# Kernel tuning notes

Hardware: AMD Instinct MI355X
Metric: run time of the kernel (lower is better)

The kernel has to match this reference:

```python
import jax, jax.numpy as jnp
import numpy as np
import math

B, T, O, D, H, L, FF = 2, 1024, 512, 1024, 16, 4, 4096
MAX_SEQ = 1024


def _ln(x, g, b, eps=1e-5):
    m = jnp.mean(x, -1, keepdims=True)
    v = jnp.mean((x - m) ** 2, -1, keepdims=True)
    return (x - m) * jax.lax.rsqrt(v + eps) * g + b


def _gelu(x):
    return jax.nn.gelu(x, approximate=False)  # torch nn.GELU default = exact erf


def setup_inputs() -> dict:
    key = jax.random.key(0)
    ks = iter(jax.random.split(key, 64))
    std = 0.02
    def w(shape):
        return (jax.random.normal(next(ks), shape, jnp.float32) * std)
    d = {
        'obs': jax.random.normal(next(ks), (B, T, O), jnp.float32),
        # encoder MLP: Linear(O,D), LN, GELU, Linear(D,D), GELU, Linear(D,D), LN
        'enc_w1': w((O, D)), 'enc_b1': jnp.zeros((D,)),
        'enc_g1': jnp.ones((D,)), 'enc_be1': jnp.zeros((D,)),
        'enc_w2': w((D, D)), 'enc_b2': jnp.zeros((D,)),
        'enc_w3': w((D, D)), 'enc_b3': jnp.zeros((D,)),
        'enc_g2': jnp.ones((D,)), 'enc_be2': jnp.zeros((D,)),
        'pos_emb': w((MAX_SEQ, D)),
        # stacked per-layer transformer params [L, ...]
        'ln1_g': jnp.ones((L, D)), 'ln1_b': jnp.zeros((L, D)),
        'wq': w((L, D, D)), 'bq': jnp.zeros((L, D)),
        'wk': w((L, D, D)), 'bk': jnp.zeros((L, D)),
        'wv': w((L, D, D)), 'bv': jnp.zeros((L, D)),
        'wo': w((L, D, D)), 'bo': jnp.zeros((L, D)),
        'ln2_g': jnp.ones((L, D)), 'ln2_b': jnp.zeros((L, D)),
        'mlp_w1': w((L, D, FF)), 'mlp_b1': jnp.zeros((L, FF)),
        'mlp_w2': w((L, FF, D)), 'mlp_b2': jnp.zeros((L, D)),
        'lnf_g': jnp.ones((D,)), 'lnf_b': jnp.zeros((D,)),
        'dec_w': w((D, O)), 'dec_b': jnp.zeros((O,)),
    }
    return d


def reference(obs, enc_w1, enc_b1, enc_g1, enc_be1, enc_w2, enc_b2, enc_w3, enc_b3,
              enc_g2, enc_be2, pos_emb, ln1_g, ln1_b, wq, bq, wk, bk, wv, bv, wo, bo,
              ln2_g, ln2_b, mlp_w1, mlp_b1, mlp_w2, mlp_b2, lnf_g, lnf_b, dec_w, dec_b):
    b, t, _ = obs.shape
    dh = D // H
    scale = 1.0 / math.sqrt(dh)
    # embedder MLP
    h = _gelu(_ln(obs @ enc_w1 + enc_b1, enc_g1, enc_be1))
    h = _gelu(h @ enc_w2 + enc_b2)
    h = _ln(h @ enc_w3 + enc_b3, enc_g2, enc_be2)
    x = h + pos_emb[:t]
    # causal mask [t, t]
    mask = jnp.tril(jnp.ones((t, t), bool))

    def block(x, p):
        g1, b1, Wq, Bq, Wk, Bk, Wv, Bv, Wo, Bo, g2, b2, W1, B1, W2, B2 = p
        hn = _ln(x, g1, b1)
        q = (hn @ Wq + Bq).reshape(b, t, H, dh).transpose(0, 2, 1, 3)
        k = (hn @ Wk + Bk).reshape(b, t, H, dh).transpose(0, 2, 1, 3)
        v = (hn @ Wv + Bv).reshape(b, t, H, dh).transpose(0, 2, 1, 3)
        att = jnp.einsum('bhtd,bhsd->bhts', q, k) * scale
        att = jnp.where(mask, att, -jnp.inf)
        att = jax.nn.softmax(att, axis=-1)
        y = jnp.einsum('bhts,bhsd->bhtd', att, v)
        y = y.transpose(0, 2, 1, 3).reshape(b, t, D)
        x = x + y @ Wo + Bo
        hm = _ln(x, g2, b2)
        x = x + _gelu(hm @ W1 + B1) @ W2 + B2
        return x, None

    stacked = (ln1_g, ln1_b, wq, bq, wk, bk, wv, bv, wo, bo,
               ln2_g, ln2_b, mlp_w1, mlp_b1, mlp_w2, mlp_b2)
    x, _ = jax.lax.scan(block, x, stacked)
    x = _ln(x, lnf_g, lnf_b)
    out_obs = x @ dec_w + dec_b
    return x, out_obs
```

## Files before the change

### kernel.cpp

```cpp
#include <hip/hip_runtime.h>

typedef unsigned short u16;
typedef __bf16  bf16x8 __attribute__((ext_vector_type(8)));
typedef float   f32x4  __attribute__((ext_vector_type(4)));
typedef unsigned short u16x4 __attribute__((ext_vector_type(4)));

constexpr int Bc = 2, Tc = 1024, Oc = 512, Dc = 1024, Hc = 16, Lc = 4, FFc = 4096;
constexpr int Mc = Bc * Tc;
constexpr int Sq = 3 * Dc;

__device__ __forceinline__ u16 f2b(float f) {
    unsigned u = __float_as_uint(f);
    u = (u + 0x7fffu + ((u >> 16) & 1u)) >> 16;
    return (u16)u;
}
__device__ __forceinline__ float gelu_f(float x) {
    return 0.5f * x * (1.0f + erff(x * 0.7071067811865476f));
}

__global__ __launch_bounds__(256) void wtrans(const float* __restrict__ in,
                                              u16* __restrict__ out, int R, int C,
                                              long inBatch, long outBatch) {
    __shared__ float t[32][33];
    const float* inp = in + (size_t)blockIdx.z * inBatch;
    u16* outp = out + (size_t)blockIdx.z * outBatch;
    const int tx = threadIdx.x & 31, ty = threadIdx.x >> 5;
    const int br = blockIdx.y * 32, bc = blockIdx.x * 32;
#pragma unroll
    for (int i = 0; i < 32; i += 8)
        t[ty + i][tx] = inp[(size_t)(br + ty + i) * C + bc + tx];
    __syncthreads();
#pragma unroll
    for (int i = 0; i < 32; i += 8)
        outp[(size_t)(bc + ty + i) * R + br + tx] = f2b(t[tx][ty + i]);
}

__global__ __launch_bounds__(256) void btrans(const u16* __restrict__ in,
                                              u16* __restrict__ out, int inStride) {
    __shared__ u16 t[32][33];
    const u16* inp = in + (size_t)blockIdx.z * Tc * inStride;
    u16* outp = out + (size_t)blockIdx.z * Dc * Tc;
    const int tx = threadIdx.x & 31, ty = threadIdx.x >> 5;
    const int br = blockIdx.y * 32, bc = blockIdx.x * 32;
#pragma unroll
    for (int i = 0; i < 32; i += 8)
        t[ty + i][tx] = inp[(size_t)(br + ty + i) * inStride + bc + tx];
    __syncthreads();
#pragma unroll
    for (int i = 0; i < 32; i += 8)
        outp[(size_t)(bc + ty + i) * Tc + br + tx] = t[tx][ty + i];
}

__global__ __launch_bounds__(256) void cvt_bf(const float* __restrict__ in,
                                              u16* __restrict__ out, int n) {
    int i = blockIdx.x * 256 + threadIdx.x;
    if (i * 4 >= n) return;
    float4 v = ((const float4*)in)[i];
    u16x4 r;
    r[0] = f2b(v.x); r[1] = f2b(v.y); r[2] = f2b(v.z); r[3] = f2b(v.w);
    ((u16x4*)out)[i] = r;
}

__global__ __launch_bounds__(256) void pack_qkv_bias(const float* __restrict__ bq,
    const float* __restrict__ bk, const float* __restrict__ bv, float* __restrict__ out) {
    int i = blockIdx.x * 256 + threadIdx.x;
    int l = i / Sq, j = i % Sq;
    float v = (j < Dc) ? bq[l * Dc + j] : (j < 2 * Dc ? bk[l * Dc + j - Dc] : bv[l * Dc + j - 2 * Dc]);
    out[i] = v;
}

__global__ __launch_bounds__(256) void ln_kernel(
    const float* __restrict__ in, const float* __restrict__ gam,
    const float* __restrict__ bet, const float* __restrict__ pos,
    float* __restrict__ outf, u16* __restrict__ outb, int do_gelu) {
    const int row = blockIdx.x, tid = threadIdx.x;
    const float4 v = ((const float4*)(in + (size_t)row * Dc))[tid];
    float s  = v.x + v.y + v.z + v.w;
    float ss = v.x * v.x + v.y * v.y + v.z * v.z + v.w * v.w;
#pragma unroll
    for (int m = 1; m < 64; m <<= 1) {
        s  += __shfl_xor(s,  m, 64);
        ss += __shfl_xor(ss, m, 64);
    }
    __shared__ float red[8];
    const int w = tid >> 6;
    if ((tid & 63) == 0) { red[w] = s; red[4 + w] = ss; }
    __syncthreads();
    s  = red[0] + red[1] + red[2] + red[3];
    ss = red[4] + red[5] + red[6] + red[7];
    const float mean = s * (1.0f / Dc);
    const float rstd = rsqrtf(ss * (1.0f / Dc) - mean * mean + 1e-5f);
    const float4 gv = ((const float4*)gam)[tid];
    const float4 bv = ((const float4*)bet)[tid];
    float y0 = (v.x - mean) * rstd * gv.x + bv.x;
    float y1 = (v.y - mean) * rstd * gv.y + bv.y;
    float y2 = (v.z - mean) * rstd * gv.z + bv.z;
    float y3 = (v.w - mean) * rstd * gv.w + bv.w;
    if (do_gelu) { y0 = gelu_f(y0); y1 = gelu_f(y1); y2 = gelu_f(y2); y3 = gelu_f(y3); }
    if (pos) {
        const float4 pv = ((const float4*)(pos + (size_t)(row & (Tc - 1)) * Dc))[tid];
        y0 += pv.x; y1 += pv.y; y2 += pv.z; y3 += pv.w;
    }
    if (outf) {
        float4 o; o.x = y0; o.y = y1; o.z = y2; o.w = y3;
        ((float4*)(outf + (size_t)row * Dc))[tid] = o;
    }
    if (outb) {
        u16x4 r; r[0] = f2b(y0); r[1] = f2b(y1); r[2] = f2b(y2); r[3] = f2b(y3);
        ((u16x4*)(outb + (size_t)row * Dc))[tid] = r;
    }
}

template<int BM, int BN, int FM, int FN, int WM, int WN, int OCC>
__global__ __launch_bounds__(256, OCC) void gemm_k(
    const u16* __restrict__ A, const u16* __restrict__ Bt,
    const float* __restrict__ bias, const float* resid,
    float* Cf, u16* Cb, int M, int N, int K, int do_gelu) {
    __shared__ u16 sA[2][BM][64];
    __shared__ u16 sB[2][BN][64];
    constexpr int NA = BM * 8 / 256;
    constexpr int NB = BN * 8 / 256;
    const int tid = threadIdx.x;
    const int lane = tid & 63, w = tid >> 6;
    const int lr = lane & 15, g = lane >> 4;
    const int wm = w / WN, wn = w % WN;

    const int gx = gridDim.x;
    const int nwg = gx * gridDim.y;
    const int orig = blockIdx.y * gx + blockIdx.x;
    const int wgid = (orig & 7) * (nwg >> 3) + (orig >> 3);
    const int bx = wgid % gx, by = wgid / gx;
    const long m0 = (long)by * BM, n0 = (long)bx * BN;

    const f32x4 fzero = {0.f, 0.f, 0.f, 0.f};
    f32x4 acc[FM][FN];
#pragma unroll
    for (int i = 0; i < FM; ++i)
#pragma unroll
        for (int j = 0; j < FN; ++j) acc[i][j] = fzero;

    bf16x8 ra[NA], rb[NB];
#pragma unroll
    for (int i = 0; i < NA; ++i) {
        int c = tid + 256 * i, row = c >> 3, cc = c & 7;
        ra[i] = *(const bf16x8*)(A + (size_t)(m0 + row) * K + cc * 8);
    }
#pragma unroll
    for (int i = 0; i < NB; ++i) {
        int c = tid + 256 * i, row = c >> 3, cc = c & 7;
        rb[i] = *(const bf16x8*)(Bt + (size_t)(n0 + row) * K + cc * 8);
    }
#pragma unroll
    for (int i = 0; i < NA; ++i) {
        int c = tid + 256 * i, row = c >> 3, cc = c & 7;
        *(bf16x8*)&sA[0][row][(cc ^ (row & 7)) * 8] = ra[i];
    }
#pragma unroll
    for (int i = 0; i < NB; ++i) {
        int c = tid + 256 * i, row = c >> 3, cc = c & 7;
        *(bf16x8*)&sB[0][row][(cc ^ (row & 7)) * 8] = rb[i];
    }
    __syncthreads();

    const int nt = K / 64;
    for (int t = 0; t < nt; ++t) {
        const int cur = t & 1;
        if (t + 1 < nt) {
            const int kk = (t + 1) * 64;
#pragma unroll
            for (int i = 0; i < NA; ++i) {
                int c = tid + 256 * i, row = c >> 3, cc = c & 7;
                ra[i] = *(const bf16x8*)(A + (size_t)(m0 + row) * K + kk + cc * 8);
            }
#pragma unroll
            for (int i = 0; i < NB; ++i) {
                int c = tid + 256 * i, row = c >> 3, cc = c & 7;
                rb[i] = *(const bf16x8*)(Bt + (size_t)(n0 + row) * K + kk + cc * 8);
            }
        }
#pragma unroll
        for (int ks = 0; ks < 2; ++ks) {
            bf16x8 fa[FM], fb[FN];
#pragma unroll
            for (int mi = 0; mi < FM; ++mi) {
                int row = wm * (16 * FM) + mi * 16 + lr;
                fa[mi] = *(const bf16x8*)&sA[cur][row][((ks * 4 + g) ^ (row & 7)) * 8];
            }
#pragma unroll
            for (int ni = 0; ni < FN; ++ni) {
                int row = wn * (16 * FN) + ni * 16 + lr;
                fb[ni] = *(const bf16x8*)&sB[cur][row][((ks * 4 + g) ^ (row & 7)) * 8];
            }
#pragma unroll
            for (int mi = 0; mi < FM; ++mi)
#pragma unroll
                for (int ni = 0; ni < FN; ++ni)
                    acc[mi][ni] = __builtin_amdgcn_mfma_f32_16x16x32_bf16(
                        fa[mi], fb[ni], acc[mi][ni], 0, 0, 0);
        }
        if (t + 1 < nt) {
            const int nxt = cur ^ 1;
#pragma unroll
            for (int i = 0; i < NA; ++i) {
                int c = tid + 256 * i, row = c >> 3, cc = c & 7;
                *(bf16x8*)&sA[nxt][row][(cc ^ (row & 7)) * 8] = ra[i];
            }
#pragma unroll
            for (int i = 0; i < NB; ++i) {
                int c = tid + 256 * i, row = c >> 3, cc = c & 7;
                *(bf16x8*)&sB[nxt][row][(cc ^ (row & 7)) * 8] = rb[i];
            }
            __syncthreads();
        }
    }
#pragma unroll
    for (int mi = 0; mi < FM; ++mi) {
#pragma unroll
        for (int ni = 0; ni < FN; ++ni) {
            const long nc = n0 + wn * (16 * FN) + ni * 16 + lr;
            const float bvv = bias ? bias[nc] : 0.0f;
#pragma unroll
            for (int j = 0; j < 4; ++j) {
                const long mr = m0 + wm * (16 * FM) + mi * 16 + g * 4 + j;
                float v = acc[mi][ni][j] + bvv;
                if (resid) v += resid[(size_t)mr * N + nc];
                if (do_gelu) v = gelu_f(v);
                if (Cf) Cf[(size_t)mr * N + nc] = v;
                if (Cb) Cb[(size_t)mr * N + nc] = f2b(v);
            }
        }
    }
}

__global__ __launch_bounds__(256, 2) void attn_kernel(
    const u16* __restrict__ qkv, const u16* __restrict__ Vt, u16* __restrict__ Yg) {
    __shared__ u16 sK[64][64];
    __shared__ u16 sV[64][64];
    __shared__ u16 sP[4][16][64];
    const int tid = threadIdx.x, w = tid >> 6, lane = tid & 63;
    const int lr = lane & 15, g = lane >> 4;
    const int hw = blockIdx.x;
    const int xcd = hw & 7, slot = hw >> 3;
    const int bh = xcd + 8 * (slot >> 4);
    const int qc = slot & 15;
    const int h = bh & 15, b = bh >> 4;
    const int tq0 = qc * 64 + w * 16;
    const u16* Qp = qkv + (size_t)b * Tc * Sq + h * 64;
    const u16* Kp = qkv + (size_t)b * Tc * Sq + Dc + h * 64;
    const u16* Vp = Vt + ((size_t)b * Dc + h * 64) * Tc;

    bf16x8 qf[2];
#pragma unroll
    for (int ks = 0; ks < 2; ++ks)
        qf[ks] = *(const bf16x8*)(Qp + (size_t)(tq0 + lr) * Sq + ks * 32 + g * 8);

    const f32x4 fzero = {0.f, 0.f, 0.f, 0.f};
    f32x4 o[4];
    float mst[4], lst[4];
#pragma unroll
    for (int j = 0; j < 4; ++j) { mst[j] = -1e30f; lst[j] = 0.f; }
#pragma unroll
    for (int ni = 0; ni < 4; ++ni) o[ni] = fzero;

    for (int jk = 0; jk <= qc; ++jk) {
#pragma unroll
        for (int i = 0; i < 2; ++i) {
            int c = tid + 256 * i;
            int row = c >> 3, cc = c & 7;
            *(bf16x8*)&sK[row][(cc ^ (row & 7)) * 8] =
                *(const bf16x8*)(Kp + (size_t)(jk * 64 + row) * Sq + cc * 8);
            *(bf16x8*)&sV[row][(cc ^ (row & 7)) * 8] =
                *(const bf16x8*)(Vp + (size_t)row * Tc + jk * 64 + cc * 8);
        }
        __syncthreads();
        f32x4 s[4];
#pragma unroll
        for (int ni = 0; ni < 4; ++ni) {
            const int row = ni * 16 + lr;
            bf16x8 kf0 = *(const bf16x8*)&sK[row][((0 + g) ^ (lr & 7)) * 8];
            bf16x8 kf1 = *(const bf16x8*)&sK[row][((4 + g) ^ (lr & 7)) * 8];
            s[ni] = __builtin_amdgcn_mfma_f32_16x16x32_bf16(qf[0], kf0, fzero, 0, 0, 0);
            s[ni] = __builtin_amdgcn_mfma_f32_16x16x32_bf16(qf[1], kf1, s[ni], 0, 0, 0);
        }
#pragma unroll
        for (int ni = 0; ni < 4; ++ni)
#pragma unroll
            for (int j = 0; j < 4; ++j) {
                float v = s[ni][j] * 0.125f;
                int tk = jk * 64 + ni * 16 + lr;
                int tq = tq0 + g * 4 + j;
                if (tk > tq) v = -1e30f;
                s[ni][j] = v;
            }
        float fs[4];
#pragma unroll
        for (int j = 0; j < 4; ++j) {
            float pm = fmaxf(fmaxf(s[0][j], s[1][j]), fmaxf(s[2][j], s[3][j]));
            pm = fmaxf(pm, __shfl_xor(pm, 1, 16));
            pm = fmaxf(pm, __shfl_xor(pm, 2, 16));
            pm = fmaxf(pm, __shfl_xor(pm, 4, 16));
            pm = fmaxf(pm, __shfl_xor(pm, 8, 16));
            const float m2 = fmaxf(mst[j], pm);
            fs[j] = __expf(mst[j] - m2);
#pragma unroll
            for (int ni = 0; ni < 4; ++ni)
                s[ni][j] = __expf(s[ni][j] - m2);
            float rsum = s[0][j] + s[1][j] + s[2][j] + s[3][j];
            rsum += __shfl_xor(rsum, 1, 16);
            rsum += __shfl_xor(rsum, 2, 16);
            rsum += __shfl_xor(rsum, 4, 16);
            rsum += __shfl_xor(rsum, 8, 16);
            lst[j] = lst[j] * fs[j] + rsum;
            mst[j] = m2;
        }
#pragma unroll
        for (int ni = 0; ni < 4; ++ni)
#pragma unroll
            for (int j = 0; j < 4; ++j) o[ni][j] *= fs[j];
#pragma unroll
        for (int ni = 0; ni < 4; ++ni)
#pragma unroll
            for (int j = 0; j < 4; ++j) {
                int row = g * 4 + j;
                int col = ni * 16 + lr;
                sP[w][row][(((col >> 3) ^ (row & 7)) << 3) | (col & 7)] = f2b(s[ni][j]);
            }
#pragma unroll
        for (int ks = 0; ks < 2; ++ks) {
            bf16x8 pf = *(const bf16x8*)&sP[w][lr][((ks * 4 + g) ^ (lr & 7)) * 8];
#pragma unroll
            for (int ni = 0; ni < 4; ++ni) {
                const int row = ni * 16 + lr;
                bf16x8 vf = *(const bf16x8*)&sV[row][((ks * 4 + g) ^ (lr & 7)) * 8];
                o[ni] = __builtin_amdgcn_mfma_f32_16x16x32_bf16(pf, vf, o[ni], 0, 0, 0);
            }
        }
        __syncthreads();
    }
#pragma unroll
    for (int ni = 0; ni < 4; ++ni)
#pragma unroll
        for (int j = 0; j < 4; ++j) {
            int tq = tq0 + g * 4 + j;
            int col = h * 64 + ni * 16 + lr;
            Yg[(size_t)(b * Tc + tq) * Dc + col] = f2b(o[ni][j] / lst[j]);
        }
}

extern "C" void kernel_launch(void* const* d_in, const int* in_sizes, int n_in,
                              void* d_out, int out_size, void* d_ws, size_t ws_size,
                              hipStream_t stream) {
    const float* obs    = (const float*)d_in[0];
    const float* enc_w1 = (const float*)d_in[1];
    const float* enc_b1 = (const float*)d_in[2];
    const float* enc_g1 = (const float*)d_in[3];
    const float* enc_be1= (const float*)d_in[4];
    const float* enc_w2 = (const float*)d_in[5];
    const float* enc_b2 = (const float*)d_in[6];
    const float* enc_w3 = (const float*)d_in[7];
    const float* enc_b3 = (const float*)d_in[8];
    const float* enc_g2 = (const float*)d_in[9];
    const float* enc_be2= (const float*)d_in[10];
    const float* pos_emb= (const float*)d_in[11];
    const float* ln1_g  = (const float*)d_in[12];
    const float* ln1_b  = (const float*)d_in[13];
    const float* wq     = (const float*)d_in[14];
    const float* bq     = (const float*)d_in[15];
    const float* wk     = (const float*)d_in[16];
    const float* bk     = (const float*)d_in[17];
    const float* wv     = (const float*)d_in[18];
    const float* bv     = (const float*)d_in[19];
    const float* wo     = (const float*)d_in[20];
    const float* bo     = (const float*)d_in[21];
    const float* ln2_g  = (const float*)d_in[22];
    const float* ln2_b  = (const float*)d_in[23];
    const float* mlp_w1 = (const float*)d_in[24];
    const float* mlp_b1 = (const float*)d_in[25];
    const float* mlp_w2 = (const float*)d_in[26];
    const float* mlp_b2 = (const float*)d_in[27];
    const float* lnf_g  = (const float*)d_in[28];
    const float* lnf_b  = (const float*)d_in[29];
    const float* dec_w  = (const float*)d_in[30];
    const float* dec_b  = (const float*)d_in[31];

    float* out_x = (float*)d_out;
    float* out_o = out_x + (size_t)Mc * Dc;

    char* base = (char*)d_ws;
    size_t off = 0;
    auto ab = [&](size_t e) -> u16* {
        u16* r = (u16*)(base + off); off += (e * 2 + 255) & ~(size_t)255; return r; };
    auto af = [&](size_t e) -> float* {
        float* r = (float*)(base + off); off += (e * 4 + 255) & ~(size_t)255; return r; };

    u16* wt_e1   = ab((size_t)Dc * Oc);
    u16* wt_e2   = ab((size_t)Dc * Dc);
    u16* wt_e3   = ab((size_t)Dc * Dc);
    u16* wtqkv   = ab((size_t)Lc * 3 * Dc * Dc);
    u16* wto     = ab((size_t)Lc * Dc * Dc);
    u16* wtm1    = ab((size_t)Lc * Dc * FFc);
    u16* wtm2    = ab((size_t)Lc * FFc * Dc);
    u16* wt_d    = ab((size_t)Oc * Dc);
    float* qkvb  = af((size_t)Lc * Sq);

    u16*   obs_bf = ab((size_t)Mc * Oc);
    float* tmpf   = af((size_t)Mc * Dc);
    float* xf     = af((size_t)Mc * Dc);
    float* x2f    = af((size_t)Mc * Dc);
    u16*   hn_bf  = ab((size_t)Mc * Dc);
    u16*   qkv    = ab((size_t)Mc * Sq);
    u16*   vT     = ab((size_t)Mc * Dc);
    u16*   y_bf   = ab((size_t)Mc * Dc);
    u16*   ff_bf  = ab((size_t)Mc * FFc);

    wtrans<<<dim3(Dc / 32, Oc / 32, 1), 256, 0, stream>>>(enc_w1, wt_e1, Oc, Dc, 0, 0);
    wtrans<<<dim3(Dc / 32, Dc / 32, 1), 256, 0, stream>>>(enc_w2, wt_e2, Dc, Dc, 0, 0);
    wtrans<<<dim3(Dc / 32, Dc / 32, 1), 256, 0, stream>>>(enc_w3, wt_e3, Dc, Dc, 0, 0);
    wtrans<<<dim3(Dc / 32, Dc / 32, Lc), 256, 0, stream>>>(wq, wtqkv,            Dc, Dc, (long)Dc * Dc, (long)3 * Dc * Dc);
    wtrans<<<dim3(Dc / 32, Dc / 32, Lc), 256, 0, stream>>>(wk, wtqkv + Dc * Dc,  Dc, Dc, (long)Dc * Dc, (long)3 * Dc * Dc);
    wtrans<<<dim3(Dc / 32, Dc / 32, Lc), 256, 0, stream>>>(wv, wtqkv + 2 * Dc * Dc, Dc, Dc, (long)Dc * Dc, (long)3 * Dc * Dc);
    wtrans<<<dim3(Dc / 32, Dc / 32, Lc), 256, 0, stream>>>(wo, wto, Dc, Dc, (long)Dc * Dc, (long)Dc * Dc);
    wtrans<<<dim3(FFc / 32, Dc / 32, Lc), 256, 0, stream>>>(mlp_w1, wtm1, Dc, FFc, (long)Dc * FFc, (long)Dc * FFc);
    wtrans<<<dim3(Dc / 32, FFc / 32, Lc), 256, 0, stream>>>(mlp_w2, wtm2, FFc, Dc, (long)Dc * FFc, (long)Dc * FFc);
    wtrans<<<dim3(Oc / 32, Dc / 32, 1), 256, 0, stream>>>(dec_w, wt_d, Dc, Oc, 0, 0);
    pack_qkv_bias<<<dim3(Lc * Sq / 256), 256, 0, stream>>>(bq, bk, bv, qkvb);
    cvt_bf<<<dim3((Mc * Oc / 4 + 255) / 256), 256, 0, stream>>>(obs, obs_bf, Mc * Oc);

    auto g128 = [&](const u16* A, const u16* Bt, const float* bias, const float* resid,
                    float* Cf, u16* Cb, int M, int N, int K, int gel) {
        gemm_k<128, 128, 4, 4, 2, 2, 2><<<dim3(N / 128, M / 128), 256, 0, stream>>>(
            A, Bt, bias, resid, Cf, Cb, M, N, K, gel);
    };
    auto g64 = [&](const u16* A, const u16* Bt, const float* bias, const float* resid,
                   float* Cf, u16* Cb, int M, int N, int K, int gel) {
        gemm_k<64, 64, 2, 2, 2, 2, 4><<<dim3(N / 64, M / 64), 256, 0, stream>>>(
            A, Bt, bias, resid, Cf, Cb, M, N, K, gel);
    };
    auto lnk = [&](const float* in, const float* gg, const float* bb, const float* pos,
                   float* outf, u16* outb, int gel) {
        ln_kernel<<<dim3(Mc), 256, 0, stream>>>(in, gg, bb, pos, outf, outb, gel);
    };

    g64(obs_bf, wt_e1, enc_b1, nullptr, tmpf, nullptr, Mc, Dc, Oc, 0);
    lnk(tmpf, enc_g1, enc_be1, nullptr, nullptr, hn_bf, 1);
    g64(hn_bf, wt_e2, enc_b2, nullptr, nullptr, y_bf, Mc, Dc, Dc, 1);
    g64(y_bf, wt_e3, enc_b3, nullptr, tmpf, nullptr, Mc, Dc, Dc, 0);
    lnk(tmpf, enc_g2, enc_be2, pos_emb, xf, nullptr, 0);

    for (int l = 0; l < Lc; ++l) {
        lnk(xf, ln1_g + (size_t)l * Dc, ln1_b + (size_t)l * Dc, nullptr, nullptr, hn_bf, 0);
        g128(hn_bf, wtqkv + (size_t)l * 3 * Dc * Dc, qkvb + (size_t)l * Sq, nullptr,
             nullptr, qkv, Mc, Sq, Dc, 0);
        btrans<<<dim3(Dc / 32, Tc / 32, Bc), 256, 0, stream>>>(qkv + 2 * Dc, vT, Sq);
        attn_kernel<<<dim3(Bc * Hc * (Tc / 64)), 256, 0, stream>>>(qkv, vT, y_bf);
        g64(y_bf, wto + (size_t)l * Dc * Dc, bo + (size_t)l * Dc, xf, x2f, nullptr, Mc, Dc, Dc, 0);
        lnk(x2f, ln2_g + (size_t)l * Dc, ln2_b + (size_t)l * Dc, nullptr, nullptr, hn_bf, 0);
        g128(hn_bf, wtm1 + (size_t)l * Dc * FFc, mlp_b1 + (size_t)l * FFc, nullptr,
             nullptr, ff_bf, Mc, FFc, Dc, 1);
        g64(ff_bf, wtm2 + (size_t)l * FFc * Dc, mlp_b2 + (size_t)l * Dc, x2f, xf, nullptr, Mc, Dc, FFc, 0);
    }

    lnk(xf, lnf_g, lnf_b, nullptr, out_x, hn_bf, 0);
    g64(hn_bf, wt_d, dec_b, nullptr, out_o, nullptr, Mc, Oc, Dc, 0);
}
```

Measured before the change: 817.1 us.

## Deepen GEMM prefetch to two register stages and split-K the MLP down-projection

The GEMM main loop now holds two register staging buffers, so global loads are issued two K-tiles ahead of compute, and the loop is unrolled by two with compile-time buffer indices. The MLP second projection (K=4096) is split into two K halves along grid z, each writing fp32 partials. A new reduction kernel then adds the partials, bias and residual. The split is meant to double the number of workgroups for that GEMM and improve occupancy. In exchange it adds extra fp32 partial traffic, an extra launch, and higher register pressure from the doubled staging arrays.

Measured after the change: 786.9 us. 3.7% less time.

```diff
diff --git a/kernel.cpp b/kernel.cpp
--- a/kernel.cpp
+++ b/kernel.cpp
@@ -1,4 +1,5 @@
 #include <hip/hip_runtime.h>
+#include <utility>
 
 typedef unsigned short u16;
 typedef __bf16  bf16x8 __attribute__((ext_vector_type(8)));
@@ -67,6 +68,21 @@
     int l = i / Sq, j = i % Sq;
     float v = (j < Dc) ? bq[l * Dc + j] : (j < 2 * Dc ? bk[l * Dc + j - Dc] : bv[l * Dc + j - 2 * Dc]);
     out[i] = v;
+}
+
+__global__ __launch_bounds__(256) void red2(const float* __restrict__ p,
+    const float* __restrict__ bias, const float* __restrict__ resid,
+    float* __restrict__ outf, int MN) {
+    const int i = blockIdx.x * 256 + threadIdx.x;
+    const f32x4 a = ((const f32x4*)p)[i];
+    const f32x4 b = ((const f32x4*)(p + MN))[i];
+    const int col4 = i & (Dc / 4 - 1);
+    const f32x4 bb = ((const f32x4*)bias)[col4];
+    const f32x4 r  = ((const f32x4*)resid)[i];
+    f32x4 o;
+#pragma unroll
+    for (int j = 0; j < 4; ++j) o[j] = a[j] + b[j] + bb[j] + r[j];
+    ((f32x4*)outf)[i] = o;
 }
 
 __global__ __launch_bounds__(256) void ln_kernel(
@@ -115,7 +131,7 @@
 __global__ __launch_bounds__(256, OCC) void gemm_k(
     const u16* __restrict__ A, const u16* __restrict__ Bt,
     const float* __restrict__ bias, const float* resid,
-    float* Cf, u16* Cb, int M, int N, int K, int do_gelu) {
+    float* Cf, u16* Cb, int M, int N, int Kst, int Kl, int do_gelu) {
     __shared__ u16 sA[2][BM][64];
     __shared__ u16 sB[2][BN][64];
     constexpr int NA = BM * 8 / 256;
@@ -125,6 +141,10 @@
     const int lr = lane & 15, g = lane >> 4;
     const int wm = w / WN, wn = w % WN;
 
+    A  += (size_t)blockIdx.z * Kl;
+    Bt += (size_t)blockIdx.z * Kl;
+    Cf += (size_t)blockIdx.z * M * N;
+
     const int gx = gridDim.x;
     const int nwg = gx * gridDim.y;
     const int orig = blockIdx.y * gx + blockIdx.x;
@@ -139,57 +159,52 @@
 #pragma unroll
         for (int j = 0; j < FN; ++j) acc[i][j] = fzero;
 
-    bf16x8 ra[NA], rb[NB];
-#pragma unroll
-    for (int i = 0; i < NA; ++i) {
-        int c = tid + 256 * i, row = c >> 3, cc = c & 7;
-        ra[i] = *(const bf16x8*)(A + (size_t)(m0 + row) * K + cc * 8);
-    }
-#pragma unroll
-    for (int i = 0; i < NB; ++i) {
-        int c = tid + 256 * i, row = c >> 3, cc = c & 7;
-        rb[i] = *(const bf16x8*)(Bt + (size_t)(n0 + row) * K + cc * 8);
-    }
-#pragma unroll
-    for (int i = 0; i < NA; ++i) {
-        int c = tid + 256 * i, row = c >> 3, cc = c & 7;
-        *(bf16x8*)&sA[0][row][(cc ^ (row & 7)) * 8] = ra[i];
-    }
-#pragma unroll
-    for (int i = 0; i < NB; ++i) {
-        int c = tid + 256 * i, row = c >> 3, cc = c & 7;
-        *(bf16x8*)&sB[0][row][(cc ^ (row & 7)) * 8] = rb[i];
-    }
-    __syncthreads();
-
-    const int nt = K / 64;
-    for (int t = 0; t < nt; ++t) {
-        const int cur = t & 1;
-        if (t + 1 < nt) {
-            const int kk = (t + 1) * 64;
+    const int nt = Kl / 64;
+    bf16x8 ra[2][NA], rb[2][NB];
+
+    auto gload = [&](auto curc, int t) {
+        constexpr int cu = decltype(curc)::value;
+        if (t < nt) {
+            const int kk = t * 64;
 #pragma unroll
             for (int i = 0; i < NA; ++i) {
                 int c = tid + 256 * i, row = c >> 3, cc = c & 7;
-                ra[i] = *(const bf16x8*)(A + (size_t)(m0 + row) * K + kk + cc * 8);
+                ra[cu][i] = *(const bf16x8*)(A + (size_t)(m0 + row) * Kst + kk + cc * 8);
             }
 #pragma unroll
             for (int i = 0; i < NB; ++i) {
                 int c = tid + 256 * i, row = c >> 3, cc = c & 7;
-                rb[i] = *(const bf16x8*)(Bt + (size_t)(n0 + row) * K + kk + cc * 8);
-            }
-        }
+                rb[cu][i] = *(const bf16x8*)(Bt + (size_t)(n0 + row) * Kst + kk + cc * 8);
+            }
+        }
+    };
+    auto lwrite = [&](auto curc) {
+        constexpr int cu = decltype(curc)::value;
+#pragma unroll
+        for (int i = 0; i < NA; ++i) {
+            int c = tid + 256 * i, row = c >> 3, cc = c & 7;
+            *(bf16x8*)&sA[cu][row][(cc ^ (row & 7)) * 8] = ra[cu][i];
+        }
+#pragma unroll
+        for (int i = 0; i < NB; ++i) {
+            int c = tid + 256 * i, row = c >> 3, cc = c & 7;
+            *(bf16x8*)&sB[cu][row][(cc ^ (row & 7)) * 8] = rb[cu][i];
+        }
+    };
+    auto compute = [&](auto curc) {
+        constexpr int cu = decltype(curc)::value;
 #pragma unroll
         for (int ks = 0; ks < 2; ++ks) {
             bf16x8 fa[FM], fb[FN];
 #pragma unroll
             for (int mi = 0; mi < FM; ++mi) {
                 int row = wm * (16 * FM) + mi * 16 + lr;
-                fa[mi] = *(const bf16x8*)&sA[cur][row][((ks * 4 + g) ^ (row & 7)) * 8];
+                fa[mi] = *(const bf16x8*)&sA[cu][row][((ks * 4 + g) ^ (row & 7)) * 8];
             }
 #pragma unroll
             for (int ni = 0; ni < FN; ++ni) {
                 int row = wn * (16 * FN) + ni * 16 + lr;
-                fb[ni] = *(const bf16x8*)&sB[cur][row][((ks * 4 + g) ^ (row & 7)) * 8];
+                fb[ni] = *(const bf16x8*)&sB[cu][row][((ks * 4 + g) ^ (row & 7)) * 8];
             }
 #pragma unroll
             for (int mi = 0; mi < FM; ++mi)
@@ -198,18 +213,23 @@
                     acc[mi][ni] = __builtin_amdgcn_mfma_f32_16x16x32_bf16(
                         fa[mi], fb[ni], acc[mi][ni], 0, 0, 0);
         }
-        if (t + 1 < nt) {
-            const int nxt = cur ^ 1;
-#pragma unroll
-            for (int i = 0; i < NA; ++i) {
-                int c = tid + 256 * i, row = c >> 3, cc = c & 7;
-                *(bf16x8*)&sA[nxt][row][(cc ^ (row & 7)) * 8] = ra[i];
-            }
-#pragma unroll
-            for (int i = 0; i < NB; ++i) {
-                int c = tid + 256 * i, row = c >> 3, cc = c & 7;
-                *(bf16x8*)&sB[nxt][row][(cc ^ (row & 7)) * 8] = rb[i];
-            }
+    };
+
+    std::integral_constant<int, 0> c0;
+    std::integral_constant<int, 1> c1;
+    gload(c0, 0);
+    gload(c1, 1);
+    lwrite(c0);
+    __syncthreads();
+    for (int t = 0; t < nt; t += 2) {
+        gload(c0, t + 2);
+        compute(c0);
+        lwrite(c1);
+        __syncthreads();
+        gload(c1, t + 3);
+        compute(c1);
+        if (t + 2 < nt) {
+            lwrite(c0);
             __syncthreads();
         }
     }
@@ -412,6 +432,7 @@
     u16*   vT     = ab((size_t)Mc * Dc);
     u16*   y_bf   = ab((size_t)Mc * Dc);
     u16*   ff_bf  = ab((size_t)Mc * FFc);
+    float* pk     = af((size_t)2 * Mc * Dc);
 
     wtrans<<<dim3(Dc / 32, Oc / 32, 1), 256, 0, stream>>>(enc_w1, wt_e1, Oc, Dc, 0, 0);
     wtrans<<<dim3(Dc / 32, Dc / 32, 1), 256, 0, stream>>>(enc_w2, wt_e2, Dc, Dc, 0, 0);
@@ -429,12 +450,12 @@
     auto g128 = [&](const u16* A, const u16* Bt, const float* bias, const float* resid,
                     float* Cf, u16* Cb, int M, int N, int K, int gel) {
         gemm_k<128, 128, 4, 4, 2, 2, 2><<<dim3(N / 128, M / 128), 256, 0, stream>>>(
-            A, Bt, bias, resid, Cf, Cb, M, N, K, gel);
+            A, Bt, bias, resid, Cf, Cb, M, N, K, K, gel);
     };
     auto g64 = [&](const u16* A, const u16* Bt, const float* bias, const float* resid,
                    float* Cf, u16* Cb, int M, int N, int K, int gel) {
         gemm_k<64, 64, 2, 2, 2, 2, 4><<<dim3(N / 64, M / 64), 256, 0, stream>>>(
-            A, Bt, bias, resid, Cf, Cb, M, N, K, gel);
+            A, Bt, bias, resid, Cf, Cb, M, N, K, K, gel);
     };
     auto lnk = [&](const float* in, const float* gg, const float* bb, const float* pos,
                    float* outf, u16* outb, int gel) {
@@ -457,7 +478,11 @@
         lnk(x2f, ln2_g + (size_t)l * Dc, ln2_b + (size_t)l * Dc, nullptr, nullptr, hn_bf, 0);
         g128(hn_bf, wtm1 + (size_t)l * Dc * FFc, mlp_b1 + (size_t)l * FFc, nullptr,
              nullptr, ff_bf, Mc, FFc, Dc, 1);
-        g64(ff_bf, wtm2 + (size_t)l * FFc * Dc, mlp_b2 + (size_t)l * Dc, x2f, xf, nullptr, Mc, Dc, FFc, 0);
+        gemm_k<64, 64, 2, 2, 2, 2, 4><<<dim3(Dc / 64, Mc / 64, 2), 256, 0, stream>>>(
+            ff_bf, wtm2 + (size_t)l * FFc * Dc, nullptr, nullptr, pk, nullptr,
+            Mc, Dc, FFc, FFc / 2, 0);
+        red2<<<dim3(Mc * Dc / 4 / 256), 256, 0, stream>>>(
+            pk, mlp_b2 + (size_t)l * Dc, x2f, xf, Mc * Dc);
     }
 
     lnk(xf, lnf_g, lnf_b, nullptr, out_x, hn_bf, 0);
```
